# Kernel optimization log

Hardware: AMD Instinct MI355X
Metric: run time of the kernel (lower is better)

## Reference

```python
import jax, jax.numpy as jnp
import numpy as np
from jax import lax

KH, KW = 3, 3  # hardcoded in the original extract_patches sizes=(1,3,3,1)


def setup_inputs() -> dict:
    key = jax.random.key(0)
    k1, k2, k3 = jax.random.split(key, 3)
    B, H, W, C = 32, 56, 56, 128
    num_och = 256
    x = jax.random.normal(k1, (B, H, W, C), dtype=jnp.float32)
    w = jax.random.normal(k2, (num_och, KH * KW * C), dtype=jnp.float32) * 0.05
    b = jax.random.normal(k3, (num_och,), dtype=jnp.float32) * 0.05
    return {"x": x, "w": w, "b": b}


def reference(x, w, b):
    # Original: extract_patches (SAME, stride 1, 3x3) -> tile num_och times ->
    # elementwise multiply with w -> reduce_sum over patch axis -> + bias.
    # This is exactly a 3x3 SAME conv: patch layout is (ky, kx, cin) row-major,
    # matching tf.image.extract_patches depth ordering.
    num_och = w.shape[0]
    cin = x.shape[-1]
    # (num_och, KH*KW*C) -> (KH, KW, C, num_och) for HWIO kernel layout
    kernel = w.reshape(num_och, KH, KW, cin).transpose(1, 2, 3, 0)
    out = lax.conv_general_dilated(
        x, kernel,
        window_strides=(1, 1),
        padding="SAME",
        dimension_numbers=("NHWC", "HWIO", "NHWC"),
    )
    return out + b
```

## Files before the change

### kernel.cpp

```cpp
#include <hip/hip_runtime.h>
#include <hip/hip_bf16.h>

#define HH   56
#define WW_  56
#define CIN  128
#define OCH  256
#define NPIX (32*56*56)
#define NX   (NPIX*CIN)
#define NW   (OCH*9*CIN)
#define XB_BYTES ((size_t)NX*2)
#define WB_BYTES ((size_t)NW*2)
#define ZP_OFF   (XB_BYTES + WB_BYTES)
#define WS_NEEDED (ZP_OFF + 256)

#define NT   18
#define SLOT 65536
#define THREADS 512

typedef __attribute__((ext_vector_type(8))) short bf16x8;
typedef __attribute__((ext_vector_type(4))) float f32x4;
typedef __attribute__((address_space(1))) void v_g;
typedef __attribute__((address_space(3))) void v_l;

__device__ __forceinline__ unsigned short f2bf(float f) {
  union { float f; unsigned u; } v; v.f = f;
  unsigned r = v.u + 0x7FFF + ((v.u >> 16) & 1);
  return (unsigned short)(r >> 16);
}

__global__ __launch_bounds__(256) void convert_kern(
    const float* __restrict__ x, const float* __restrict__ w,
    char* __restrict__ ws)
{
  if (blockIdx.x == 0 && threadIdx.x < 64)
    ((float*)(ws + ZP_OFF))[threadIdx.x] = 0.f;

  unsigned short* out = (unsigned short*)ws;
  const int NT8 = (NX + NW) / 8;
  for (int i = blockIdx.x * blockDim.x + threadIdx.x; i < NT8;
       i += gridDim.x * blockDim.x) {
    const int e = i * 8;
    const float* src = (e < NX) ? (x + e) : (w + (e - NX));
    const float4 a = ((const float4*)src)[0];
    const float4 b = ((const float4*)src)[1];
    union { bf16x8 v; unsigned short u[8]; } p;
    p.u[0] = f2bf(a.x); p.u[1] = f2bf(a.y); p.u[2] = f2bf(a.z); p.u[3] = f2bf(a.w);
    p.u[4] = f2bf(b.x); p.u[5] = f2bf(b.y); p.u[6] = f2bf(b.z); p.u[7] = f2bf(b.w);
    *(bf16x8*)(out + e) = p.v;
  }
}

__global__ __launch_bounds__(THREADS, 2) void conv_gemm5(
    const char* __restrict__ ws, const float* __restrict__ bias,
    float* __restrict__ out)
{
  __shared__ char lds[2 * SLOT];

  const char* xb = ws;
  const char* wb = ws + XB_BYTES;
  const char* zp = ws + ZP_OFF;

  const int tid  = threadIdx.x;
  const int lane = tid & 63;

  const int bid = blockIdx.x;
  const int m0  = ((bid & 7) * 49 + (bid >> 3)) * 256;

  const int r0  = tid >> 3;
  const int chk = ((tid & 7) ^ (r0 & 7)) * 16;
  const char* zpc = zp + chk;

  int pixA[4], phA[4], pwA[4];
  const char* bsrc[4];
#pragma unroll
  for (int l = 0; l < 4; ++l) {
    const int r  = r0 + l * 64;
    const int p  = m0 + r;
    const int pb = p / 3136;
    const int phw = p - pb * 3136;
    phA[l] = phw / 56;
    pwA[l] = phw - phA[l] * 56;
    pixA[l] = p;
    bsrc[l] = wb + (size_t)r * 2304 + chk;
  }

  const int fr = lane & 15;
  const int fq = lane >> 4;
  const int wv = tid >> 6;
  const int wr = wv >> 2;
  const int wc = wv & 3;

  int aoffs[8], boffs[4];
#pragma unroll
  for (int mi = 0; mi < 8; ++mi) {
    const int r = wr * 128 + mi * 16 + fr;
    aoffs[mi] = r * 128 + ((fq * 16) ^ ((r & 7) << 4));
  }
#pragma unroll
  for (int nj = 0; nj < 4; ++nj) {
    const int c = wc * 64 + nj * 16 + fr;
    boffs[nj] = 32768 + c * 128 + ((fq * 16) ^ ((c & 7) << 4));
  }

  f32x4 acc[8][4];
  const f32x4 zero4 = {0.f, 0.f, 0.f, 0.f};
#pragma unroll
  for (int mi = 0; mi < 8; ++mi)
#pragma unroll
    for (int nj = 0; nj < 4; ++nj) acc[mi][nj] = zero4;

#define STAGE(tt, dst) do {                                                   \
    const int kpos_ = (tt) >> 1, kh_ = (tt) & 1;                              \
    const int ky_ = kpos_ / 3;                                                \
    const int dy_ = ky_ - 1, dx_ = kpos_ - ky_ * 3 - 1;                       \
    _Pragma("unroll")                                                         \
    for (int l = 0; l < 4; ++l) {                                             \
      const int ih_ = phA[l] + dy_, iw_ = pwA[l] + dx_;                       \
      const bool v_ = ((unsigned)ih_ < 56u) & ((unsigned)iw_ < 56u);          \
      const char* ga_ = v_ ? (xb + (size_t)(pixA[l] + dy_ * 56 + dx_) * 256   \
                                 + kh_ * 128 + chk)                           \
                           : zpc;                                             \
      __builtin_amdgcn_global_load_lds((const v_g*)ga_,                       \
          (v_l*)((dst) + l * 8192 + tid * 16), 16, 0, 0);                     \
    }                                                                         \
    _Pragma("unroll")                                                         \
    for (int l = 0; l < 4; ++l)                                               \
      __builtin_amdgcn_global_load_lds((const v_g*)(bsrc[l] + (tt) * 128),    \
          (v_l*)((dst) + 32768 + l * 8192 + tid * 16), 16, 0, 0);             \
  } while (0)

#define COMPUTE(src) do {                                                     \
    _Pragma("unroll")                                                         \
    for (int ks = 0; ks < 2; ++ks) {                                          \
      bf16x8 Af[8], Bf[4];                                                    \
      _Pragma("unroll")                                                       \
      for (int mi = 0; mi < 8; ++mi)                                          \
        Af[mi] = *(const bf16x8*)((src) + (aoffs[mi] ^ (ks << 6)));           \
      _Pragma("unroll")                                                       \
      for (int nj = 0; nj < 4; ++nj)                                          \
        Bf[nj] = *(const bf16x8*)((src) + (boffs[nj] ^ (ks << 6)));           \
      __builtin_amdgcn_s_setprio(1);                                          \
      _Pragma("unroll")                                                       \
      for (int mi = 0; mi < 8; ++mi)                                          \
        _Pragma("unroll")                                                     \
        for (int nj = 0; nj < 4; ++nj)                                        \
          acc[mi][nj] = __builtin_amdgcn_mfma_f32_16x16x32_bf16(              \
              Af[mi], Bf[nj], acc[mi][nj], 0, 0, 0);                          \
      __builtin_amdgcn_s_setprio(0);                                          \
    }                                                                         \
  } while (0)

  char* s0 = lds;
  char* s1 = lds + SLOT;

  STAGE(0, s0);

#pragma unroll
  for (int t = 0; t < NT - 1; ++t) {
    __builtin_amdgcn_s_barrier();
    __builtin_amdgcn_sched_barrier(0);
    STAGE(t + 1, ((t + 1) & 1) ? s1 : s0);
    asm volatile("s_waitcnt vmcnt(8)" ::: "memory");
    __builtin_amdgcn_s_barrier();
    __builtin_amdgcn_sched_barrier(0);
    COMPUTE((t & 1) ? s1 : s0);
  }

  asm volatile("s_waitcnt vmcnt(0)" ::: "memory");
  __builtin_amdgcn_s_barrier();
  __builtin_amdgcn_sched_barrier(0);
  COMPUTE(((NT - 1) & 1) ? s1 : s0);

#undef STAGE
#undef COMPUTE

  float bv[4];
#pragma unroll
  for (int nj = 0; nj < 4; ++nj) bv[nj] = bias[wc * 64 + nj * 16 + fr];

#pragma unroll
  for (int mi = 0; mi < 8; ++mi) {
#pragma unroll
    for (int j = 0; j < 4; ++j) {
      const int prow = m0 + wr * 128 + mi * 16 + fq * 4 + j;
      float* orow = out + (size_t)prow * OCH + wc * 64 + fr;
#pragma unroll
      for (int nj = 0; nj < 4; ++nj)
        orow[nj * 16] = acc[mi][nj][j] + bv[nj];
    }
  }
}

__global__ __launch_bounds__(256) void conv3x3_mfma_fb(
    const float* __restrict__ x, const float* __restrict__ w,
    const float* __restrict__ bias, float* __restrict__ out)
{
  __shared__ alignas(16) unsigned char As[128 * 64];
  __shared__ alignas(16) unsigned char Bs[128 * 64];

  const int tid = threadIdx.x;
  const int m0 = (blockIdx.x >> 1) * 128;
  const int n0 = (blockIdx.x & 1) * 128;

  const int srow = tid >> 1;
  const int soff = (tid & 1) * 16;

  const int p   = m0 + srow;
  const int pb  = p / (HH * WW_);
  const int phw = p - pb * (HH * WW_);
  const int ph  = phw / WW_;
  const int pw  = phw - ph * WW_;

  const float* xrow = x + ((size_t)((pb * HH + ph) * WW_ + pw)) * CIN + soff;
  const float* wrow = w + (size_t)(n0 + srow) * (9 * CIN) + soff;

  const int sw0 = (srow * 64 + soff * 2)      ^ ((srow & 7) << 4);
  const int sw1 = (srow * 64 + soff * 2 + 16) ^ ((srow & 7) << 4);

  const int lane = tid & 63;
  const int wv = tid >> 6;
  const int wm = (wv >> 1) * 64;
  const int wn = (wv & 1) * 64;
  const int fr = lane & 15;
  const int fq = lane >> 4;

  int aoff[4], boff[4];
#pragma unroll
  for (int i = 0; i < 4; ++i) {
    const int r = wm + i * 16 + fr;
    aoff[i] = (r * 64 + fq * 16) ^ ((r & 7) << 4);
    const int c = wn + i * 16 + fr;
    boff[i] = (c * 64 + fq * 16) ^ ((c & 7) << 4);
  }

  f32x4 acc[4][4];
  const f32x4 zero4 = {0.f, 0.f, 0.f, 0.f};
#pragma unroll
  for (int i = 0; i < 4; ++i)
#pragma unroll
    for (int j = 0; j < 4; ++j) acc[i][j] = zero4;

#pragma unroll 1
  for (int kpos = 0; kpos < 9; ++kpos) {
    const int ky = kpos / 3;
    const int kx = kpos - ky * 3;
    const int ih = ph + ky - 1;
    const int iw = pw + kx - 1;
    const bool valid = ((unsigned)ih < (unsigned)HH) & ((unsigned)iw < (unsigned)WW_);
    const float* asrc = xrow + ((ky - 1) * WW_ + (kx - 1)) * CIN;
    const float* bsrc2 = wrow + kpos * CIN;

#pragma unroll 1
    for (int kc = 0; kc < 4; ++kc) {
      float4 a0, a1, a2, a3;
      if (valid) {
        const float4* s = (const float4*)(asrc + kc * 32);
        a0 = s[0]; a1 = s[1]; a2 = s[2]; a3 = s[3];
      } else {
        a0 = make_float4(0.f, 0.f, 0.f, 0.f);
        a1 = a0; a2 = a0; a3 = a0;
      }
      const float4* tql = (const float4*)(bsrc2 + kc * 32);
      const float4 b0 = tql[0], b1 = tql[1], b2 = tql[2], b3 = tql[3];

      __syncthreads();

      union { bf16x8 v; unsigned short u[8]; } pA0, pA1, pB0, pB1;
      pA0.u[0] = f2bf(a0.x); pA0.u[1] = f2bf(a0.y); pA0.u[2] = f2bf(a0.z); pA0.u[3] = f2bf(a0.w);
      pA0.u[4] = f2bf(a1.x); pA0.u[5] = f2bf(a1.y); pA0.u[6] = f2bf(a1.z); pA0.u[7] = f2bf(a1.w);
      pA1.u[0] = f2bf(a2.x); pA1.u[1] = f2bf(a2.y); pA1.u[2] = f2bf(a2.z); pA1.u[3] = f2bf(a2.w);
      pA1.u[4] = f2bf(a3.x); pA1.u[5] = f2bf(a3.y); pA1.u[6] = f2bf(a3.z); pA1.u[7] = f2bf(a3.w);
      pB0.u[0] = f2bf(b0.x); pB0.u[1] = f2bf(b0.y); pB0.u[2] = f2bf(b0.z); pB0.u[3] = f2bf(b0.w);
      pB0.u[4] = f2bf(b1.x); pB0.u[5] = f2bf(b1.y); pB0.u[6] = f2bf(b1.z); pB0.u[7] = f2bf(b1.w);
      pB1.u[0] = f2bf(b2.x); pB1.u[1] = f2bf(b2.y); pB1.u[2] = f2bf(b2.z); pB1.u[3] = f2bf(b2.w);
      pB1.u[4] = f2bf(b3.x); pB1.u[5] = f2bf(b3.y); pB1.u[6] = f2bf(b3.z); pB1.u[7] = f2bf(b3.w);

      *(bf16x8*)(As + sw0) = pA0.v;
      *(bf16x8*)(As + sw1) = pA1.v;
      *(bf16x8*)(Bs + sw0) = pB0.v;
      *(bf16x8*)(Bs + sw1) = pB1.v;

      __syncthreads();

      bf16x8 af[4], bfr[4];
#pragma unroll
      for (int i = 0; i < 4; ++i) af[i]  = *(const bf16x8*)(As + aoff[i]);
#pragma unroll
      for (int j = 0; j < 4; ++j) bfr[j] = *(const bf16x8*)(Bs + boff[j]);
#pragma unroll
      for (int i = 0; i < 4; ++i)
#pragma unroll
        for (int j = 0; j < 4; ++j)
          acc[i][j] = __builtin_amdgcn_mfma_f32_16x16x32_bf16(af[i], bfr[j], acc[i][j], 0, 0, 0);
    }
  }

  float bv[4];
#pragma unroll
  for (int j = 0; j < 4; ++j) bv[j] = bias[n0 + wn + j * 16 + fr];

#pragma unroll
  for (int mi = 0; mi < 4; ++mi) {
#pragma unroll
    for (int j = 0; j < 4; ++j) {
      const int prow = m0 + wm + mi * 16 + fq * 4 + j;
      float* orow = out + (size_t)prow * OCH + n0 + wn + fr;
#pragma unroll
      for (int ni = 0; ni < 4; ++ni)
        orow[ni * 16] = acc[mi][ni][j] + bv[ni];
    }
  }
}

extern "C" void kernel_launch(void* const* d_in, const int* in_sizes, int n_in,
                              void* d_out, int out_size, void* d_ws, size_t ws_size,
                              hipStream_t stream) {
  (void)in_sizes; (void)n_in; (void)out_size;
  const float* x = (const float*)d_in[0];
  const float* w = (const float*)d_in[1];
  const float* b = (const float*)d_in[2];
  float* out = (float*)d_out;

  if (ws_size >= WS_NEEDED) {
    convert_kern<<<dim3(2048), dim3(256), 0, stream>>>(x, w, (char*)d_ws);
    const int grid = NPIX / 256;
    conv_gemm5<<<dim3(grid), dim3(THREADS), 0, stream>>>((const char*)d_ws, b, out);
  } else {
    conv3x3_mfma_fb<<<dim3((NPIX / 128) * 2), dim3(256), 0, stream>>>(x, w, b, out);
  }
}
```

Measured before the change: 206.1 us.

## Split MFMA compute into four barrier-synchronized phases interleaving LDS reads

Splits each tile's compute into four phases. Each phase loads half of the A fragments (and the B fragments on alternate phases) from LDS, then runs a 4x4 block of MFMAs, with workgroup barriers around each phase. The leading barrier of the main loop is removed, since the trailing barrier of the last phase now protects the buffer before it is restaged. The goal is to keep waves in lockstep so LDS reads and MFMA work overlap across waves, and to lower register pressure by holding fewer A fragments at once. In exchange there are many more barriers per tile.

```diff
diff --git a/kernel.cpp b/kernel.cpp
--- a/kernel.cpp
+++ b/kernel.cpp
@@ -50,7 +50,7 @@
   }
 }
 
-__global__ __launch_bounds__(THREADS, 2) void conv_gemm5(
+__global__ __launch_bounds__(THREADS, 2) void conv_gemm6(
     const char* __restrict__ ws, const float* __restrict__ bias,
     float* __restrict__ out)
 {
@@ -129,25 +129,37 @@
           (v_l*)((dst) + 32768 + l * 8192 + tid * 16), 16, 0, 0);             \
   } while (0)
 
+#define PHASE(src, ks, mq, LOADB) do {                                        \
+    bf16x8 Aq[4];                                                             \
+    _Pragma("unroll")                                                         \
+    for (int i = 0; i < 4; ++i)                                               \
+      Aq[i] = *(const bf16x8*)((src) + (aoffs[(mq) * 4 + i] ^ ((ks) << 6)));  \
+    if (LOADB) {                                                              \
+      _Pragma("unroll")                                                       \
+      for (int j = 0; j < 4; ++j)                                             \
+        Bq[j] = *(const bf16x8*)((src) + (boffs[j] ^ ((ks) << 6)));           \
+    }                                                                         \
+    __builtin_amdgcn_sched_barrier(0);                                        \
+    __builtin_amdgcn_s_barrier();                                             \
+    __builtin_amdgcn_sched_barrier(0);                                        \
+    __builtin_amdgcn_s_setprio(1);                                            \
+    _Pragma("unroll")                                                         \
+    for (int i = 0; i < 4; ++i)                                               \
+      _Pragma("unroll")                                                       \
+      for (int j = 0; j < 4; ++j)                                             \
+        acc[(mq) * 4 + i][j] = __builtin_amdgcn_mfma_f32_16x16x32_bf16(       \
+            Aq[i], Bq[j], acc[(mq) * 4 + i][j], 0, 0, 0);                     \
+    __builtin_amdgcn_s_setprio(0);                                            \
+    __builtin_amdgcn_sched_barrier(0);                                        \
+    __builtin_amdgcn_s_barrier();                                             \
+  } while (0)
+
 #define COMPUTE(src) do {                                                     \
-    _Pragma("unroll")                                                         \
-    for (int ks = 0; ks < 2; ++ks) {                                          \
-      bf16x8 Af[8], Bf[4];                                                    \
-      _Pragma("unroll")                                                       \
-      for (int mi = 0; mi < 8; ++mi)                                          \
-        Af[mi] = *(const bf16x8*)((src) + (aoffs[mi] ^ (ks << 6)));           \
-      _Pragma("unroll")                                                       \
-      for (int nj = 0; nj < 4; ++nj)                                          \
-        Bf[nj] = *(const bf16x8*)((src) + (boffs[nj] ^ (ks << 6)));           \
-      __builtin_amdgcn_s_setprio(1);                                          \
-      _Pragma("unroll")                                                       \
-      for (int mi = 0; mi < 8; ++mi)                                          \
-        _Pragma("unroll")                                                     \
-        for (int nj = 0; nj < 4; ++nj)                                        \
-          acc[mi][nj] = __builtin_amdgcn_mfma_f32_16x16x32_bf16(              \
-              Af[mi], Bf[nj], acc[mi][nj], 0, 0, 0);                          \
-      __builtin_amdgcn_s_setprio(0);                                          \
-    }                                                                         \
+    bf16x8 Bq[4];                                                             \
+    PHASE(src, 0, 0, true);                                                   \
+    PHASE(src, 0, 1, false);                                                  \
+    PHASE(src, 1, 0, true);                                                   \
+    PHASE(src, 1, 1, false);                                                  \
   } while (0)
 
   char* s0 = lds;
@@ -157,8 +169,6 @@
 
 #pragma unroll
   for (int t = 0; t < NT - 1; ++t) {
-    __builtin_amdgcn_s_barrier();
-    __builtin_amdgcn_sched_barrier(0);
     STAGE(t + 1, ((t + 1) & 1) ? s1 : s0);
     asm volatile("s_waitcnt vmcnt(8)" ::: "memory");
     __builtin_amdgcn_s_barrier();
@@ -172,6 +182,7 @@
   COMPUTE(((NT - 1) & 1) ? s1 : s0);
 
 #undef STAGE
+#undef PHASE
 #undef COMPUTE
 
   float bv[4];
@@ -324,7 +335,7 @@
   if (ws_size >= WS_NEEDED) {
     convert_kern<<<dim3(2048), dim3(256), 0, stream>>>(x, w, (char*)d_ws);
     const int grid = NPIX / 256;
-    conv_gemm5<<<dim3(grid), dim3(THREADS), 0, stream>>>((const char*)d_ws, b, out);
+    conv_gemm6<<<dim3(grid), dim3(THREADS), 0, stream>>>((const char*)d_ws, b, out);
   } else {
     conv3x3_mfma_fb<<<dim3((NPIX / 128) * 2), dim3(256), 0, stream>>>(x, w, b, out);
   }
```

Measured after the change: 207.7 us. No clear change (+0.8%).
